# Kernel optimization log

Hardware: AMD Instinct MI355X
Metric: run time of the kernel (lower is better)

Reference implementation:

```python
import jax, jax.numpy as jnp
import numpy as np

B, T, D = 128, 1024, 128
HS = [100, 100, 200, 200]  # stacked LSTM hidden sizes (from initialize_carry calls)
OUT = 6


def _lstm_layer(xs, Wx, Wh, b):
    """Flax-style LSTMCell scanned over time. xs: [B,T,Din] -> [B,T,H].
    Gates: i,f,g,o ; c' = sig(f)*c + sig(i)*tanh(g) ; h' = sig(o)*tanh(c')."""
    Bsz = xs.shape[0]
    H = Wh.shape[0]
    c0 = jnp.zeros((Bsz, H), xs.dtype)
    h0 = jnp.zeros((Bsz, H), xs.dtype)

    def step(carry, x_t):
        c, h = carry
        z = x_t @ Wx + h @ Wh + b  # [B, 4H]
        i, f, g, o = jnp.split(z, 4, axis=-1)
        c = jax.nn.sigmoid(f) * c + jax.nn.sigmoid(i) * jnp.tanh(g)
        h = jax.nn.sigmoid(o) * jnp.tanh(c)
        return (c, h), h

    (_, _), hs = jax.lax.scan(step, (c0, h0), jnp.swapaxes(xs, 0, 1))  # hs: [T,B,H]
    return jnp.swapaxes(hs, 0, 1)


def setup_inputs() -> dict:
    key = jax.random.key(0)
    ks = jax.random.split(key, 16)
    xs = jax.random.normal(ks[0], (B, T, D), dtype=jnp.float32)
    inp = {"xs": xs}
    d_in = D
    for li, H in enumerate(HS):
        s_x = 1.0 / np.sqrt(d_in)
        s_h = 1.0 / np.sqrt(H)
        inp[f"Wx{li}"] = jax.random.normal(ks[1 + 3 * li], (d_in, 4 * H), dtype=jnp.float32) * s_x
        inp[f"Wh{li}"] = jax.random.normal(ks[2 + 3 * li], (H, 4 * H), dtype=jnp.float32) * s_h
        inp[f"b{li}"] = jnp.zeros((4 * H,), dtype=jnp.float32)
        d_in = H
    inp["Wd"] = jax.random.normal(ks[13], (HS[-1], OUT), dtype=jnp.float32) / np.sqrt(HS[-1])
    inp["bd"] = jnp.zeros((OUT,), dtype=jnp.float32)
    return inp


def reference(xs, Wx0, Wh0, b0, Wx1, Wh1, b1, Wx2, Wh2, b2, Wx3, Wh3, b3, Wd, bd):
    # Four stacked scanned LSTM layers (dropout is identity in eval mode)
    h = _lstm_layer(xs, Wx0, Wh0, b0)
    h = _lstm_layer(h, Wx1, Wh1, b1)
    h = _lstm_layer(h, Wx2, Wh2, b2)
    h = _lstm_layer(h, Wx3, Wh3, b3)
    last = h[:, -1, :]  # [B, 200]
    return last @ Wd + bd  # [B, 6]
```

## Files before the change

### kernel.cpp

```cpp
#include <hip/hip_runtime.h>
#include <cstdint>
#include <cstddef>


#define AGENT __HIP_MEMORY_SCOPE_AGENT
#define FSTR 64

typedef __attribute__((ext_vector_type(8))) short  short8;
typedef __attribute__((ext_vector_type(4))) float  f32x4;

struct us4 { unsigned short x, y, z, w; };

__device__ __forceinline__ unsigned short f2bf(float x){
  unsigned u = __float_as_uint(x);
  unsigned r = u + 0x7FFFu + ((u >> 16) & 1u);
  return (unsigned short)(r >> 16);
}
__device__ __forceinline__ float bf2f(unsigned short h){
  return __uint_as_float(((unsigned)h) << 16);
}
__device__ __forceinline__ float sigmoidf_(float x){ return 1.f / (1.f + __expf(-x)); }

__device__ __forceinline__ void spin_ge(const unsigned* p, unsigned v){
  #pragma unroll 1
  for (int i = 0; i < 32; ++i){
    if (__hip_atomic_load(p, __ATOMIC_RELAXED, AGENT) >= v) return;
  }
  long s = 0;
  #pragma unroll 1
  while (__hip_atomic_load(p, __ATOMIC_RELAXED, AGENT) < v){
    __builtin_amdgcn_s_sleep(8);
    if (++s > (1L << 17)) break;
  }
}

__device__ __forceinline__ void load_hx(const unsigned* base, int w32, int loOff,
                                        short8& ah, short8& al){
  union U { unsigned long long q[2]; short8 v; } uh, ul;
  const unsigned long long* ph = (const unsigned long long*)(base + w32);
  const unsigned long long* pl = (const unsigned long long*)(base + loOff + w32);
  uh.q[0] = __hip_atomic_load(ph + 0, __ATOMIC_RELAXED, AGENT);
  uh.q[1] = __hip_atomic_load(ph + 1, __ATOMIC_RELAXED, AGENT);
  ul.q[0] = __hip_atomic_load(pl + 0, __ATOMIC_RELAXED, AGENT);
  ul.q[1] = __hip_atomic_load(pl + 1, __ATOMIC_RELAXED, AGENT);
  ah = uh.v; al = ul.v;
}

__global__ __launch_bounds__(256) void gemm_pregate(
    const float* __restrict__ A, const float* __restrict__ W,
    const float* __restrict__ bias, float* __restrict__ G,
    int K, int KT, int N, size_t strideT, size_t strideB)
{
  __shared__ unsigned short Ahi[256*40];
  __shared__ unsigned short Alo[256*40];
  __shared__ unsigned short Bhi[80*40];
  __shared__ unsigned short Blo[80*40];

  const int tid  = threadIdx.x;
  const int mb   = blockIdx.x;
  const int n0   = blockIdx.y * 80;
  const int wave = tid >> 6, lane = tid & 63;
  const int ln15 = lane & 15, quad = lane >> 4;

  f32x4 acc[4][5];
  for (int a = 0; a < 4; ++a)
    for (int b = 0; b < 5; ++b)
      acc[a][b] = (f32x4){0.f, 0.f, 0.f, 0.f};

  for (int kt = 0; kt < KT; ++kt){
    const int k0 = kt * 32;
    const bool full = (k0 + 31) < K;
    for (int i = 0; i < 8; ++i){
      const int e   = tid + 256*i;
      const int row = e >> 3, seg = e & 7;
      const int mm  = mb*256 + row;
      const float* rp = A + (size_t)(mm >> 7)*strideT + (size_t)(mm & 127)*strideB;
      const int k = k0 + seg*4;
      float v0, v1, v2, v3;
      if (full){
        float4 v = *(const float4*)(rp + k);
        v0 = v.x; v1 = v.y; v2 = v.z; v3 = v.w;
      } else {
        v0 = (k+0 < K) ? rp[k+0] : 0.f;
        v1 = (k+1 < K) ? rp[k+1] : 0.f;
        v2 = (k+2 < K) ? rp[k+2] : 0.f;
        v3 = (k+3 < K) ? rp[k+3] : 0.f;
      }
      const unsigned short h0=f2bf(v0), h1=f2bf(v1), h2=f2bf(v2), h3=f2bf(v3);
      us4 hv{h0, h1, h2, h3};
      us4 lv{f2bf(v0-bf2f(h0)), f2bf(v1-bf2f(h1)), f2bf(v2-bf2f(h2)), f2bf(v3-bf2f(h3))};
      *(us4*)&Ahi[row*40 + seg*4] = hv;
      *(us4*)&Alo[row*40 + seg*4] = lv;
    }
    for (int i = 0; i < 10; ++i){
      const int e  = tid + 256*i;
      const int kk = e / 80, nn = e - kk*80;
      const int k  = k0 + kk;
      const float v = (k < K) ? W[(size_t)k*N + n0 + nn] : 0.f;
      const unsigned short hb = f2bf(v);
      Bhi[nn*40 + kk] = hb;
      Blo[nn*40 + kk] = f2bf(v - bf2f(hb));
    }
    __syncthreads();
    short8 a_h[4], a_l[4];
    for (int mt = 0; mt < 4; ++mt){
      const int aoff = (wave*64 + mt*16 + ln15)*40 + quad*8;
      a_h[mt] = *(const short8*)&Ahi[aoff];
      a_l[mt] = *(const short8*)&Alo[aoff];
    }
    for (int nt = 0; nt < 5; ++nt){
      const int boff = (nt*16 + ln15)*40 + quad*8;
      const short8 b_h = *(const short8*)&Bhi[boff];
      const short8 b_l = *(const short8*)&Blo[boff];
      for (int mt = 0; mt < 4; ++mt){
        acc[mt][nt] = __builtin_amdgcn_mfma_f32_16x16x32_bf16(a_h[mt], b_h, acc[mt][nt], 0,0,0);
        acc[mt][nt] = __builtin_amdgcn_mfma_f32_16x16x32_bf16(a_l[mt], b_h, acc[mt][nt], 0,0,0);
        acc[mt][nt] = __builtin_amdgcn_mfma_f32_16x16x32_bf16(a_h[mt], b_l, acc[mt][nt], 0,0,0);
      }
    }
    __syncthreads();
  }
  for (int nt = 0; nt < 5; ++nt){
    const float bv = bias[n0 + nt*16 + ln15];
    for (int mt = 0; mt < 4; ++mt){
      const int mbase = mb*256 + wave*64 + mt*16 + quad*4;
      #pragma unroll
      for (int r = 0; r < 4; ++r)
        G[(size_t)(mbase + r)*N + n0 + nt*16 + ln15] = acc[mt][nt][r] + bv;
    }
  }
}

template<int H, int HP, int P, bool HAS_X>
__device__ __forceinline__ void rec_stage(
    const float* __restrict__ G0, const float* __restrict__ Wx,
    const float* __restrict__ Wh, const float* __restrict__ bias,
    int HprevReal,
    const unsigned* __restrict__ HxUp, unsigned* __restrict__ HxOwn,
    const unsigned* __restrict__ flgUp, unsigned* __restrict__ flgOwn,
    unsigned* __restrict__ flgDn, int PUp, int PDn,
    float* __restrict__ cstate, float* __restrict__ hlast,
    int g, int m, int t0, int TC, int Tlast, char* smem)
{
  constexpr int HHM  = H / P;
  constexpr int COLS = 4 * HHM;
  constexpr int CP   = COLS;
  constexpr int ZSTR = CP + 1;
  constexpr int KPo  = ((H + 31)/32)*32;
  constexpr int RSo  = KPo / 2;
  constexpr int RSp  = HP / 2;
  constexpr int KX   = HAS_X ? HP : 0;
  constexpr int KALL = KX + KPo;
  constexpr int KTX  = KX / 32;
  constexpr int KTH  = KPo / 32;
  constexpr int KSTR = KALL + 8;
  constexpr int NT   = CP / 16;
  constexpr int NE   = 16 * HHM / 2;
  constexpr int PR   = HHM / 2;
  constexpr int N4H  = 4 * H;
  constexpr int SLOTo = 2*16*RSo;
  constexpr int SLOTp = 2*16*RSp;

  unsigned short* whT_hi = (unsigned short*)smem;
  unsigned short* whT_lo = whT_hi + CP*KSTR;
  float* zbuf = (float*)(whT_lo + CP*KSTR);

  const int tid  = threadIdx.x;
  const int row0 = g * 16;
  const int lane = tid & 63, wave = tid >> 6;
  const int ln15 = lane & 15, quad = lane >> 4;

  for (int e = tid; e < COLS*KALL; e += 256){
    const int k = e / COLS, c = e - k*COLS;
    const int gate = c / HHM, hh = c - gate*HHM;
    const int col = gate*H + m*HHM + hh;
    float w = 0.f;
    if (HAS_X){
      if (k < KX){ if (k < HprevReal) w = Wx[(size_t)k*N4H + col]; }
      else { const int k2 = k - KX; if (k2 < H) w = Wh[(size_t)k2*N4H + col]; }
    } else {
      if (k < H) w = Wh[(size_t)k*N4H + col];
    }
    const unsigned short hi = f2bf(w);
    whT_hi[c*KSTR + k] = hi;
    whT_lo[c*KSTR + k] = f2bf(w - bf2f(hi));
  }

  const int r_g  = tid / PR;
  const int hh0  = 2*(tid - r_g*PR);
  const int kidx = m*HHM + hh0;
  float c0 = 0.f, c1 = 0.f;
  if (tid < NE && t0 > 0){
    const float2 cv = *(const float2*)&cstate[(size_t)(row0 + r_g)*H + kidx];
    c0 = cv.x; c1 = cv.y;
  }
  float2 bv[4] = {};
  if (HAS_X){
    if (tid < NE){
      #pragma unroll
      for (int gate = 0; gate < 4; ++gate)
        bv[gate] = *(const float2*)&bias[gate*H + kidx];
    }
  }
  __syncthreads();

  const int g16 = g*16;

  for (int tl = 0; tl < TC; ++tl){
    const int t = t0 + tl;

    float2 gv[4] = {};
    if constexpr (!HAS_X){
      if (tid < NE){
        const float* Gt = G0 + ((size_t)tl*128 + row0 + r_g)*(size_t)N4H + kidx;
        #pragma unroll
        for (int gate = 0; gate < 4; ++gate)
          gv[gate] = *(const float2*)(Gt + gate*H);
      }
    }

    if (HAS_X && lane < PUp)
      spin_ge(&flgUp[(size_t)(g16 + lane)*FSTR], (unsigned)(t+1));
    __builtin_amdgcn_fence(__ATOMIC_ACQUIRE, "wavefront");

    f32x4 acc[2];
    acc[0] = (f32x4){0.f,0.f,0.f,0.f};
    acc[1] = (f32x4){0.f,0.f,0.f,0.f};
    auto do_tile = [&](const short8& a_h, const short8& a_l, int koW){
      #pragma unroll
      for (int s = 0; s < 2; ++s){
        const int nt = wave + 4*s;
        if (nt < NT){
          const int boff = (nt*16 + ln15)*KSTR + quad*8 + koW;
          const short8 b_h = *(const short8*)&whT_hi[boff];
          const short8 b_l = *(const short8*)&whT_lo[boff];
          acc[s] = __builtin_amdgcn_mfma_f32_16x16x32_bf16(a_h, b_h, acc[s], 0,0,0);
          acc[s] = __builtin_amdgcn_mfma_f32_16x16x32_bf16(a_l, b_h, acc[s], 0,0,0);
          acc[s] = __builtin_amdgcn_mfma_f32_16x16x32_bf16(a_h, b_l, acc[s], 0,0,0);
        }
      }
    };

    if constexpr (HAS_X){
      const unsigned* up = HxUp + ((size_t)(t & 7)*8 + g) * SLOTp;
      #pragma unroll
      for (int kt = 0; kt < KTX; ++kt){
        short8 a_h, a_l;
        load_hx(up, ln15*RSp + kt*16 + quad*4, 16*RSp, a_h, a_l);
        do_tile(a_h, a_l, kt*32);
      }
    }

    if (lane < P && lane != m)
      spin_ge(&flgOwn[(size_t)(g16 + lane)*FSTR], (unsigned)t);
    if (PDn > 0 && t >= 8 && lane >= 40 && lane < 40 + PDn)
      spin_ge(&flgDn[(size_t)(g16 + (lane-40))*FSTR], (unsigned)(t-7));
    __builtin_amdgcn_fence(__ATOMIC_ACQUIRE, "wavefront");

    {
      const unsigned* own = HxOwn + ((size_t)((t-1) & 7)*8 + g) * SLOTo;
      #pragma unroll
      for (int kt = 0; kt < KTH; ++kt){
        short8 a_h, a_l;
        load_hx(own, ln15*RSo + kt*16 + quad*4, 16*RSo, a_h, a_l);
        do_tile(a_h, a_l, KX + kt*32);
      }
    }
    {
      #pragma unroll
      for (int s = 0; s < 2; ++s){
        const int nt = wave + 4*s;
        if (nt < NT)
          #pragma unroll
          for (int r = 0; r < 4; ++r)
            zbuf[(quad*4 + r)*ZSTR + nt*16 + ln15] = acc[s][r];
      }
    }
    __syncthreads();

    if (tid < NE){
      const float* zr = zbuf + r_g*ZSTR;
      const float2 b0 = HAS_X ? bv[0] : gv[0];
      const float2 b1 = HAS_X ? bv[1] : gv[1];
      const float2 b2 = HAS_X ? bv[2] : gv[2];
      const float2 b3 = HAS_X ? bv[3] : gv[3];
      const float zi0 = zr[0*HHM + hh0]   + b0.x, zi1 = zr[0*HHM + hh0+1] + b0.y;
      const float zf0 = zr[1*HHM + hh0]   + b1.x, zf1 = zr[1*HHM + hh0+1] + b1.y;
      const float zg0 = zr[2*HHM + hh0]   + b2.x, zg1 = zr[2*HHM + hh0+1] + b2.y;
      const float zo0 = zr[3*HHM + hh0]   + b3.x, zo1 = zr[3*HHM + hh0+1] + b3.y;
      c0 = sigmoidf_(zf0)*c0 + sigmoidf_(zi0)*tanhf(zg0);
      c1 = sigmoidf_(zf1)*c1 + sigmoidf_(zi1)*tanhf(zg1);
      const float h0 = sigmoidf_(zo0)*tanhf(c0);
      const float h1 = sigmoidf_(zo1)*tanhf(c1);
      const unsigned short h0h = f2bf(h0), h1h = f2bf(h1);
      const unsigned short h0l = f2bf(h0 - bf2f(h0h)), h1l = f2bf(h1 - bf2f(h1h));
      const unsigned whi = ((unsigned)h1h << 16) | (unsigned)h0h;
      const unsigned wlo = ((unsigned)h1l << 16) | (unsigned)h0l;
      unsigned* dst = HxOwn + ((size_t)(t & 7)*8 + g) * SLOTo;
      const int w32 = r_g*RSo + (kidx >> 1);
      __hip_atomic_store(&dst[w32],          whi, __ATOMIC_RELAXED, AGENT);
      __hip_atomic_store(&dst[16*RSo + w32], wlo, __ATOMIC_RELAXED, AGENT);
      if (hlast && t == Tlast-1){
        float2 hv{h0, h1};
        *(float2*)&hlast[(size_t)(row0 + r_g)*H + kidx] = hv;
      }
    }
    __syncthreads();
    if (tid == 0)
      __hip_atomic_store(&flgOwn[(size_t)(g16 + m)*FSTR], (unsigned)(t+1),
                         __ATOMIC_RELAXED, AGENT);
  }

  if (tid < NE){
    float2 cv{c0, c1};
    *(float2*)&cstate[(size_t)(row0 + r_g)*H + kidx] = cv;
  }
}

struct FusedArgs {
  const float *G0;
  const float *Wx1, *Wx2, *Wx3;
  const float *Wh0, *Wh1, *Wh2, *Wh3;
  const float *b1, *b2, *b3;
  unsigned *Hx0, *Hx1, *Hx2, *Hx3;
  unsigned *flags;
  float *cst;
  float *hlast;
  int t0, TC, Tlast;
};

__global__ __launch_bounds__(256) void lstm_fused(FusedArgs a){
  extern __shared__ char smem[];
  const int b = blockIdx.x;
  constexpr int LF = 128*FSTR;
  if (b < 40){
    rec_stage<100, 0, 5, false>(a.G0, nullptr, a.Wh0, nullptr, 0,
        nullptr, a.Hx0, nullptr, a.flags + 0*LF, a.flags + 1*LF, 0, 5,
        a.cst + 0*128*200, nullptr, b & 7, b >> 3, a.t0, a.TC, a.Tlast, smem);
  } else if (b < 80){
    const int bb = b - 40;
    rec_stage<100, 128, 5, true>(nullptr, a.Wx1, a.Wh1, a.b1, 100,
        a.Hx0, a.Hx1, a.flags + 0*LF, a.flags + 1*LF, a.flags + 2*LF, 5, 10,
        a.cst + 1*128*200, nullptr, bb & 7, bb >> 3, a.t0, a.TC, a.Tlast, smem);
  } else if (b < 160){
    const int bb = b - 80;
    rec_stage<200, 128, 10, true>(nullptr, a.Wx2, a.Wh2, a.b2, 100,
        a.Hx1, a.Hx2, a.flags + 1*LF, a.flags + 2*LF, a.flags + 3*LF, 5, 10,
        a.cst + 2*128*200, nullptr, bb & 7, bb >> 3, a.t0, a.TC, a.Tlast, smem);
  } else {
    const int bb = b - 160;
    rec_stage<200, 224, 10, true>(nullptr, a.Wx3, a.Wh3, a.b3, 200,
        a.Hx2, a.Hx3, a.flags + 2*LF, a.flags + 3*LF, nullptr, 10, 0,
        a.cst + 3*128*200, a.hlast, bb & 7, bb >> 3, a.t0, a.TC, a.Tlast, smem);
  }
}

__global__ __launch_bounds__(256) void head_kernel(
    const float* __restrict__ hlast, const float* __restrict__ Wd,
    const float* __restrict__ bd, float* __restrict__ out)
{
  const int e = blockIdx.x*256 + threadIdx.x;
  if (e >= 128*6) return;
  const int b = e / 6, o = e - 6*b;
  float s = bd[o];
  const float* hp = hlast + (size_t)b*200;
  for (int k = 0; k < 200; ++k) s += hp[k] * Wd[k*6 + o];
  out[e] = s;
}

__global__ void fill_sentinel(float* out, int n){
  const int i = blockIdx.x*blockDim.x + threadIdx.x;
  if (i < n) out[i] = 1.0e30f;
}

extern "C" void kernel_launch(void* const* d_in, const int* in_sizes, int n_in,
                              void* d_out, int out_size, void* d_ws, size_t ws_size,
                              hipStream_t stream)
{
  (void)in_sizes; (void)n_in;
  const float* xs  = (const float*)d_in[0];
  const float* Wx[4] = {(const float*)d_in[1], (const float*)d_in[4],
                        (const float*)d_in[7], (const float*)d_in[10]};
  const float* Wh[4] = {(const float*)d_in[2], (const float*)d_in[5],
                        (const float*)d_in[8], (const float*)d_in[11]};
  const float* bs[4] = {(const float*)d_in[3], (const float*)d_in[6],
                        (const float*)d_in[9], (const float*)d_in[12]};
  const float* Wd = (const float*)d_in[13];
  const float* bd = (const float*)d_in[14];
  float* out = (float*)d_out;

  char* ws = (char*)d_ws;
  const size_t HXU[4] = {131072, 131072, 229376, 229376};
  const size_t HX_TOT = HXU[0]+HXU[1]+HXU[2]+HXU[3];
  const size_t FLAGS_BYTES = (size_t)4*128*FSTR*4;
  size_t off = 0;
  const size_t OFF_FLAGS = off; off += FLAGS_BYTES;
  const size_t OFF_HX    = off; off += HX_TOT*4;
  const size_t OFF_CST   = off; off += (size_t)4*128*200*4;
  const size_t OFF_HLAST = off; off += (size_t)128*200*4;
  off = (off + 255) & ~(size_t)255;
  const size_t FIXED_END = off;

  int CT = 0;
  for (int ct = 1024; ct >= 8; ct >>= 1){
    const size_t need = FIXED_END + (size_t)ct*128*400*4;
    if (ws_size >= need){ CT = ct; break; }
  }
  if (CT == 0){
    fill_sentinel<<<(out_size + 255)/256, 256, 0, stream>>>(out, out_size);
    return;
  }

  unsigned* flags = (unsigned*)(ws + OFF_FLAGS);
  unsigned* Hx0   = (unsigned*)(ws + OFF_HX);
  unsigned* Hx1   = Hx0 + HXU[0];
  unsigned* Hx2   = Hx1 + HXU[1];
  unsigned* Hx3   = Hx2 + HXU[2];
  float* cst      = (float*)(ws + OFF_CST);
  float* hlast    = (float*)(ws + OFF_HLAST);
  float* G0       = (float*)(ws + FIXED_END);

  const int FUSED_LDS = 151104;
  hipFuncSetAttribute(reinterpret_cast<const void*>(lstm_fused),
                      hipFuncAttributeMaxDynamicSharedMemorySize, FUSED_LDS);

  hipMemsetAsync(flags, 0, FLAGS_BYTES, stream);
  hipMemsetAsync(Hx0, 0, HX_TOT*4, stream);

  FusedArgs fa;
  fa.Wx1 = Wx[1]; fa.Wx2 = Wx[2]; fa.Wx3 = Wx[3];
  fa.Wh0 = Wh[0]; fa.Wh1 = Wh[1]; fa.Wh2 = Wh[2]; fa.Wh3 = Wh[3];
  fa.b1 = bs[1];  fa.b2 = bs[2];  fa.b3 = bs[3];
  fa.Hx0 = Hx0; fa.Hx1 = Hx1; fa.Hx2 = Hx2; fa.Hx3 = Hx3;
  fa.flags = flags; fa.cst = cst; fa.hlast = hlast;
  fa.G0 = G0; fa.Tlast = 1024;

  const int NC  = 1024 / CT;
  const int GMX = CT*128/256;
  for (int c = 0; c < NC; ++c){
    const int t0 = c*CT;
    gemm_pregate<<<dim3(GMX,5), 256, 0, stream>>>(xs + (size_t)t0*128, Wx[0], bs[0], G0,
        128, 4, 400, (size_t)128, (size_t)131072);
    fa.t0 = t0; fa.TC = CT;
    lstm_fused<<<240, 256, FUSED_LDS, stream>>>(fa);
  }

  head_kernel<<<3, 256, 0, stream>>>(hlast, Wd, bd, out);
}
```

Baseline: 6.474 ms.

## Merge per-step flag spins into one wave-wide wait and use fast tanh

Folds the three separate spin-waits (upstream layer, own peer blocks, downstream back-pressure) into a single per-lane spin whose pointer and offset are chosen once before the time loop, so all waits run concurrently instead of one after another. All A operands (upstream and own hidden state) are then loaded up front into register arrays before the MFMA loop. This loses the earlier overlap of upstream-input MFMAs with the wait on sibling blocks, and it raises register pressure. It also swaps tanhf for an exp-based formula, which is cheaper but slightly less accurate.

```diff
diff --git a/kernel.cpp b/kernel.cpp
--- a/kernel.cpp
+++ b/kernel.cpp
@@ -20,6 +20,9 @@
   return __uint_as_float(((unsigned)h) << 16);
 }
 __device__ __forceinline__ float sigmoidf_(float x){ return 1.f / (1.f + __expf(-x)); }
+__device__ __forceinline__ float tanhf_(float x){
+  return 1.f - 2.f / (1.f + __expf(2.f * x));
+}
 
 __device__ __forceinline__ void spin_ge(const unsigned* p, unsigned v){
   #pragma unroll 1
@@ -153,6 +156,7 @@
   constexpr int KALL = KX + KPo;
   constexpr int KTX  = KX / 32;
   constexpr int KTH  = KPo / 32;
+  constexpr int NTL  = KTX + KTH;
   constexpr int KSTR = KALL + 8;
   constexpr int NT   = CP / 16;
   constexpr int NE   = 16 * HHM / 2;
@@ -206,6 +210,18 @@
 
   const int g16 = g*16;
 
+  const unsigned* spin_p = nullptr;
+  int spin_dv = 0;
+  bool spin_bp = false;
+  if (HAS_X && lane < PUp){
+    spin_p = &flgUp[(size_t)(g16 + lane)*FSTR]; spin_dv = 1;
+  } else if (lane >= 16 && lane < 16 + P && (lane - 16) != m){
+    spin_p = &flgOwn[(size_t)(g16 + lane - 16)*FSTR]; spin_dv = 0;
+  } else if (PDn > 0 && lane >= 40 && lane < 40 + PDn){
+    spin_p = &flgDn[(size_t)(g16 + lane - 40)*FSTR]; spin_dv = -7;
+    spin_bp = true;
+  }
+
   for (int tl = 0; tl < TC; ++tl){
     const int t = t0 + tl;
 
@@ -219,62 +235,49 @@
       }
     }
 
-    if (HAS_X && lane < PUp)
-      spin_ge(&flgUp[(size_t)(g16 + lane)*FSTR], (unsigned)(t+1));
+    if (spin_p && !(spin_bp && t < 8))
+      spin_ge(spin_p, (unsigned)(t + spin_dv));
     __builtin_amdgcn_fence(__ATOMIC_ACQUIRE, "wavefront");
+
+    short8 ah[NTL], al[NTL];
+    if constexpr (HAS_X){
+      const unsigned* up = HxUp + ((size_t)(t & 7)*8 + g) * SLOTp;
+      #pragma unroll
+      for (int kt = 0; kt < KTX; ++kt)
+        load_hx(up, ln15*RSp + kt*16 + quad*4, 16*RSp, ah[kt], al[kt]);
+    }
+    {
+      const unsigned* own = HxOwn + ((size_t)((t-1) & 7)*8 + g) * SLOTo;
+      #pragma unroll
+      for (int kt = 0; kt < KTH; ++kt)
+        load_hx(own, ln15*RSo + kt*16 + quad*4, 16*RSo, ah[KTX+kt], al[KTX+kt]);
+    }
 
     f32x4 acc[2];
     acc[0] = (f32x4){0.f,0.f,0.f,0.f};
     acc[1] = (f32x4){0.f,0.f,0.f,0.f};
-    auto do_tile = [&](const short8& a_h, const short8& a_l, int koW){
+    #pragma unroll
+    for (int kt = 0; kt < NTL; ++kt){
       #pragma unroll
       for (int s = 0; s < 2; ++s){
         const int nt = wave + 4*s;
         if (nt < NT){
-          const int boff = (nt*16 + ln15)*KSTR + quad*8 + koW;
+          const int boff = (nt*16 + ln15)*KSTR + quad*8 + kt*32;
           const short8 b_h = *(const short8*)&whT_hi[boff];
           const short8 b_l = *(const short8*)&whT_lo[boff];
-          acc[s] = __builtin_amdgcn_mfma_f32_16x16x32_bf16(a_h, b_h, acc[s], 0,0,0);
-          acc[s] = __builtin_amdgcn_mfma_f32_16x16x32_bf16(a_l, b_h, acc[s], 0,0,0);
-          acc[s] = __builtin_amdgcn_mfma_f32_16x16x32_bf16(a_h, b_l, acc[s], 0,0,0);
+          acc[s] = __builtin_amdgcn_mfma_f32_16x16x32_bf16(ah[kt], b_h, acc[s], 0,0,0);
+          acc[s] = __builtin_amdgcn_mfma_f32_16x16x32_bf16(al[kt], b_h, acc[s], 0,0,0);
+          acc[s] = __builtin_amdgcn_mfma_f32_16x16x32_bf16(ah[kt], b_l, acc[s], 0,0,0);
         }
       }
-    };
-
-    if constexpr (HAS_X){
-      const unsigned* up = HxUp + ((size_t)(t & 7)*8 + g) * SLOTp;
-      #pragma unroll
-      for (int kt = 0; kt < KTX; ++kt){
-        short8 a_h, a_l;
-        load_hx(up, ln15*RSp + kt*16 + quad*4, 16*RSp, a_h, a_l);
-        do_tile(a_h, a_l, kt*32);
-      }
-    }
-
-    if (lane < P && lane != m)
-      spin_ge(&flgOwn[(size_t)(g16 + lane)*FSTR], (unsigned)t);
-    if (PDn > 0 && t >= 8 && lane >= 40 && lane < 40 + PDn)
-      spin_ge(&flgDn[(size_t)(g16 + (lane-40))*FSTR], (unsigned)(t-7));
-    __builtin_amdgcn_fence(__ATOMIC_ACQUIRE, "wavefront");
-
-    {
-      const unsigned* own = HxOwn + ((size_t)((t-1) & 7)*8 + g) * SLOTo;
-      #pragma unroll
-      for (int kt = 0; kt < KTH; ++kt){
-        short8 a_h, a_l;
-        load_hx(own, ln15*RSo + kt*16 + quad*4, 16*RSo, a_h, a_l);
-        do_tile(a_h, a_l, KX + kt*32);
-      }
-    }
-    {
-      #pragma unroll
-      for (int s = 0; s < 2; ++s){
-        const int nt = wave + 4*s;
-        if (nt < NT)
-          #pragma unroll
-          for (int r = 0; r < 4; ++r)
-            zbuf[(quad*4 + r)*ZSTR + nt*16 + ln15] = acc[s][r];
-      }
+    }
+    #pragma unroll
+    for (int s = 0; s < 2; ++s){
+      const int nt = wave + 4*s;
+      if (nt < NT)
+        #pragma unroll
+        for (int r = 0; r < 4; ++r)
+          zbuf[(quad*4 + r)*ZSTR + nt*16 + ln15] = acc[s][r];
     }
     __syncthreads();
 
@@ -288,10 +291,10 @@
       const float zf0 = zr[1*HHM + hh0]   + b1.x, zf1 = zr[1*HHM + hh0+1] + b1.y;
       const float zg0 = zr[2*HHM + hh0]   + b2.x, zg1 = zr[2*HHM + hh0+1] + b2.y;
       const float zo0 = zr[3*HHM + hh0]   + b3.x, zo1 = zr[3*HHM + hh0+1] + b3.y;
-      c0 = sigmoidf_(zf0)*c0 + sigmoidf_(zi0)*tanhf(zg0);
-      c1 = sigmoidf_(zf1)*c1 + sigmoidf_(zi1)*tanhf(zg1);
-      const float h0 = sigmoidf_(zo0)*tanhf(c0);
-      const float h1 = sigmoidf_(zo1)*tanhf(c1);
+      c0 = sigmoidf_(zf0)*c0 + sigmoidf_(zi0)*tanhf_(zg0);
+      c1 = sigmoidf_(zf1)*c1 + sigmoidf_(zi1)*tanhf_(zg1);
+      const float h0 = sigmoidf_(zo0)*tanhf_(c0);
+      const float h1 = sigmoidf_(zo1)*tanhf_(c1);
       const unsigned short h0h = f2bf(h0), h1h = f2bf(h1);
       const unsigned short h0l = f2bf(h0 - bf2f(h0h)), h1l = f2bf(h1 - bf2f(h1h));
       const unsigned whi = ((unsigned)h1h << 16) | (unsigned)h0h;
```

Result: slower. 7.491 ms (+15.7%).

## Replace per-block flags with per-group atomic counters and reorder recurrent MFMA before upstream wait

Applied to the files above, without the earlier changes.

Replaces the per-block step flags with one atomic counter per (layer, batch group), incremented by every producing block, so a single lane polls one counter instead of many lanes polling separate flags. The own-layer recurrent h·Wh tiles are now issued before waiting on the upstream and downstream counters, so that work can overlap the upstream layer's progress. The change also swaps tanhf for an exp-based fast tanh and shortens the spin sleep while raising the iteration cap. Risks include reduced tanh accuracy, memory-ordering subtleties since the atomics are relaxed, and counters that must be reset correctly across chunked launches.

```diff
diff --git a/kernel.cpp b/kernel.cpp
--- a/kernel.cpp
+++ b/kernel.cpp
@@ -20,6 +20,9 @@
   return __uint_as_float(((unsigned)h) << 16);
 }
 __device__ __forceinline__ float sigmoidf_(float x){ return 1.f / (1.f + __expf(-x)); }
+__device__ __forceinline__ float tanhf_(float x){
+  return 1.f - 2.f / (1.f + __expf(2.f * x));
+}
 
 __device__ __forceinline__ void spin_ge(const unsigned* p, unsigned v){
   #pragma unroll 1
@@ -29,8 +32,8 @@
   long s = 0;
   #pragma unroll 1
   while (__hip_atomic_load(p, __ATOMIC_RELAXED, AGENT) < v){
-    __builtin_amdgcn_s_sleep(8);
-    if (++s > (1L << 17)) break;
+    __builtin_amdgcn_s_sleep(2);
+    if (++s > (1L << 19)) break;
   }
 }
 
@@ -137,8 +140,8 @@
     const float* __restrict__ Wh, const float* __restrict__ bias,
     int HprevReal,
     const unsigned* __restrict__ HxUp, unsigned* __restrict__ HxOwn,
-    const unsigned* __restrict__ flgUp, unsigned* __restrict__ flgOwn,
-    unsigned* __restrict__ flgDn, int PUp, int PDn,
+    const unsigned* __restrict__ ctrUp, unsigned* __restrict__ ctrOwn,
+    const unsigned* __restrict__ ctrDn, int PUp, int PDn,
     float* __restrict__ cstate, float* __restrict__ hlast,
     int g, int m, int t0, int TC, int Tlast, char* smem)
 {
@@ -204,7 +207,12 @@
   }
   __syncthreads();
 
-  const int g16 = g*16;
+  const unsigned* cOwn = ctrOwn + (size_t)g*FSTR;
+  unsigned*       cOwnW = ctrOwn + (size_t)g*FSTR;
+  const unsigned* cUp  = HAS_X  ? (ctrUp + (size_t)g*FSTR) : nullptr;
+  const unsigned* cDn  = (PDn>0) ? (ctrDn + (size_t)g*FSTR) : nullptr;
+  const bool isUpLane = (HAS_X && lane == 0);
+  const bool isDnLane = (PDn > 0 && lane == 32);
 
   for (int tl = 0; tl < TC; ++tl){
     const int t = t0 + tl;
@@ -219,8 +227,8 @@
       }
     }
 
-    if (HAS_X && lane < PUp)
-      spin_ge(&flgUp[(size_t)(g16 + lane)*FSTR], (unsigned)(t+1));
+    if (lane == 0)
+      spin_ge(cOwn, (unsigned)(P * t));
     __builtin_amdgcn_fence(__ATOMIC_ACQUIRE, "wavefront");
 
     f32x4 acc[2];
@@ -241,6 +249,27 @@
       }
     };
 
+    {
+      const unsigned* own = HxOwn + ((size_t)((t-1) & 7)*8 + g) * SLOTo;
+      #pragma unroll
+      for (int kt = 0; kt < KTH; ++kt){
+        short8 a_h, a_l;
+        load_hx(own, ln15*RSo + kt*16 + quad*4, 16*RSo, a_h, a_l);
+        do_tile(a_h, a_l, KX + kt*32);
+      }
+    }
+
+    {
+      const bool act = (isUpLane) || (isDnLane && t >= 8);
+      if (act){
+        const unsigned* p2 = isUpLane ? cUp : cDn;
+        const unsigned tgt = isUpLane ? (unsigned)(PUp * (t+1))
+                                      : (unsigned)(PDn * (t-7));
+        spin_ge(p2, tgt);
+      }
+    }
+    __builtin_amdgcn_fence(__ATOMIC_ACQUIRE, "wavefront");
+
     if constexpr (HAS_X){
       const unsigned* up = HxUp + ((size_t)(t & 7)*8 + g) * SLOTp;
       #pragma unroll
@@ -251,21 +280,6 @@
       }
     }
 
-    if (lane < P && lane != m)
-      spin_ge(&flgOwn[(size_t)(g16 + lane)*FSTR], (unsigned)t);
-    if (PDn > 0 && t >= 8 && lane >= 40 && lane < 40 + PDn)
-      spin_ge(&flgDn[(size_t)(g16 + (lane-40))*FSTR], (unsigned)(t-7));
-    __builtin_amdgcn_fence(__ATOMIC_ACQUIRE, "wavefront");
-
-    {
-      const unsigned* own = HxOwn + ((size_t)((t-1) & 7)*8 + g) * SLOTo;
-      #pragma unroll
-      for (int kt = 0; kt < KTH; ++kt){
-        short8 a_h, a_l;
-        load_hx(own, ln15*RSo + kt*16 + quad*4, 16*RSo, a_h, a_l);
-        do_tile(a_h, a_l, KX + kt*32);
-      }
-    }
     {
       #pragma unroll
       for (int s = 0; s < 2; ++s){
@@ -288,10 +302,10 @@
       const float zf0 = zr[1*HHM + hh0]   + b1.x, zf1 = zr[1*HHM + hh0+1] + b1.y;
       const float zg0 = zr[2*HHM + hh0]   + b2.x, zg1 = zr[2*HHM + hh0+1] + b2.y;
       const float zo0 = zr[3*HHM + hh0]   + b3.x, zo1 = zr[3*HHM + hh0+1] + b3.y;
-      c0 = sigmoidf_(zf0)*c0 + sigmoidf_(zi0)*tanhf(zg0);
-      c1 = sigmoidf_(zf1)*c1 + sigmoidf_(zi1)*tanhf(zg1);
-      const float h0 = sigmoidf_(zo0)*tanhf(c0);
-      const float h1 = sigmoidf_(zo1)*tanhf(c1);
+      c0 = sigmoidf_(zf0)*c0 + sigmoidf_(zi0)*tanhf_(zg0);
+      c1 = sigmoidf_(zf1)*c1 + sigmoidf_(zi1)*tanhf_(zg1);
+      const float h0 = sigmoidf_(zo0)*tanhf_(c0);
+      const float h1 = sigmoidf_(zo1)*tanhf_(c1);
       const unsigned short h0h = f2bf(h0), h1h = f2bf(h1);
       const unsigned short h0l = f2bf(h0 - bf2f(h0h)), h1l = f2bf(h1 - bf2f(h1h));
       const unsigned whi = ((unsigned)h1h << 16) | (unsigned)h0h;
@@ -307,8 +321,7 @@
     }
     __syncthreads();
     if (tid == 0)
-      __hip_atomic_store(&flgOwn[(size_t)(g16 + m)*FSTR], (unsigned)(t+1),
-                         __ATOMIC_RELAXED, AGENT);
+      __hip_atomic_fetch_add(cOwnW, 1u, __ATOMIC_RELAXED, AGENT);
   }
 
   if (tid < NE){
@@ -332,25 +345,26 @@
 __global__ __launch_bounds__(256) void lstm_fused(FusedArgs a){
   extern __shared__ char smem[];
   const int b = blockIdx.x;
-  constexpr int LF = 128*FSTR;
+  constexpr int LF = 8*FSTR;
+  unsigned* F = a.flags;
   if (b < 40){
     rec_stage<100, 0, 5, false>(a.G0, nullptr, a.Wh0, nullptr, 0,
-        nullptr, a.Hx0, nullptr, a.flags + 0*LF, a.flags + 1*LF, 0, 5,
+        nullptr, a.Hx0, nullptr, F + 0*LF, F + 1*LF, 0, 5,
         a.cst + 0*128*200, nullptr, b & 7, b >> 3, a.t0, a.TC, a.Tlast, smem);
   } else if (b < 80){
     const int bb = b - 40;
     rec_stage<100, 128, 5, true>(nullptr, a.Wx1, a.Wh1, a.b1, 100,
-        a.Hx0, a.Hx1, a.flags + 0*LF, a.flags + 1*LF, a.flags + 2*LF, 5, 10,
+        a.Hx0, a.Hx1, F + 0*LF, F + 1*LF, F + 2*LF, 5, 10,
         a.cst + 1*128*200, nullptr, bb & 7, bb >> 3, a.t0, a.TC, a.Tlast, smem);
   } else if (b < 160){
     const int bb = b - 80;
     rec_stage<200, 128, 10, true>(nullptr, a.Wx2, a.Wh2, a.b2, 100,
-        a.Hx1, a.Hx2, a.flags + 1*LF, a.flags + 2*LF, a.flags + 3*LF, 5, 10,
+        a.Hx1, a.Hx2, F + 1*LF, F + 2*LF, F + 3*LF, 5, 10,
         a.cst + 2*128*200, nullptr, bb & 7, bb >> 3, a.t0, a.TC, a.Tlast, smem);
   } else {
     const int bb = b - 160;
     rec_stage<200, 224, 10, true>(nullptr, a.Wx3, a.Wh3, a.b3, 200,
-        a.Hx2, a.Hx3, a.flags + 2*LF, a.flags + 3*LF, nullptr, 10, 0,
+        a.Hx2, a.Hx3, F + 2*LF, F + 3*LF, nullptr, 10, 0,
         a.cst + 3*128*200, a.hlast, bb & 7, bb >> 3, a.t0, a.TC, a.Tlast, smem);
   }
 }
@@ -392,7 +406,7 @@
   char* ws = (char*)d_ws;
   const size_t HXU[4] = {131072, 131072, 229376, 229376};
   const size_t HX_TOT = HXU[0]+HXU[1]+HXU[2]+HXU[3];
-  const size_t FLAGS_BYTES = (size_t)4*128*FSTR*4;
+  const size_t FLAGS_BYTES = (size_t)4*8*FSTR*4;
   size_t off = 0;
   const size_t OFF_FLAGS = off; off += FLAGS_BYTES;
   const size_t OFF_HX    = off; off += HX_TOT*4;
```

Result: slower. 7.867 ms (+21.5%).

## Fuse layer-0 input projection into recurrent kernel, drop pregate GEMM

Applied to the files above, without the earlier changes.

Removes the separate pregate GEMM for layer 0. Layer-0 blocks now load xs directly each timestep, split it into bf16 hi/lo parts and multiply by Wx0 held in LDS alongside Wh0, which leaves a single fused launch over all 1024 steps with no G0 workspace. It also replaces tanhf with an exp-based tanh. This avoids the extra kernel, the G0 write/read traffic and any chunking, at the cost of more per-step work and global xs loads on layer 0's critical path.

```diff
diff --git a/kernel.cpp b/kernel.cpp
--- a/kernel.cpp
+++ b/kernel.cpp
@@ -8,8 +8,6 @@
 
 typedef __attribute__((ext_vector_type(8))) short  short8;
 typedef __attribute__((ext_vector_type(4))) float  f32x4;
-
-struct us4 { unsigned short x, y, z, w; };
 
 __device__ __forceinline__ unsigned short f2bf(float x){
   unsigned u = __float_as_uint(x);
@@ -20,6 +18,9 @@
   return __uint_as_float(((unsigned)h) << 16);
 }
 __device__ __forceinline__ float sigmoidf_(float x){ return 1.f / (1.f + __expf(-x)); }
+__device__ __forceinline__ float tanhf_(float x){
+  return 1.f - 2.f / (1.f + __expf(2.f * x));
+}
 
 __device__ __forceinline__ void spin_ge(const unsigned* p, unsigned v){
   #pragma unroll 1
@@ -46,96 +47,11 @@
   ah = uh.v; al = ul.v;
 }
 
-__global__ __launch_bounds__(256) void gemm_pregate(
-    const float* __restrict__ A, const float* __restrict__ W,
-    const float* __restrict__ bias, float* __restrict__ G,
-    int K, int KT, int N, size_t strideT, size_t strideB)
-{
-  __shared__ unsigned short Ahi[256*40];
-  __shared__ unsigned short Alo[256*40];
-  __shared__ unsigned short Bhi[80*40];
-  __shared__ unsigned short Blo[80*40];
-
-  const int tid  = threadIdx.x;
-  const int mb   = blockIdx.x;
-  const int n0   = blockIdx.y * 80;
-  const int wave = tid >> 6, lane = tid & 63;
-  const int ln15 = lane & 15, quad = lane >> 4;
-
-  f32x4 acc[4][5];
-  for (int a = 0; a < 4; ++a)
-    for (int b = 0; b < 5; ++b)
-      acc[a][b] = (f32x4){0.f, 0.f, 0.f, 0.f};
-
-  for (int kt = 0; kt < KT; ++kt){
-    const int k0 = kt * 32;
-    const bool full = (k0 + 31) < K;
-    for (int i = 0; i < 8; ++i){
-      const int e   = tid + 256*i;
-      const int row = e >> 3, seg = e & 7;
-      const int mm  = mb*256 + row;
-      const float* rp = A + (size_t)(mm >> 7)*strideT + (size_t)(mm & 127)*strideB;
-      const int k = k0 + seg*4;
-      float v0, v1, v2, v3;
-      if (full){
-        float4 v = *(const float4*)(rp + k);
-        v0 = v.x; v1 = v.y; v2 = v.z; v3 = v.w;
-      } else {
-        v0 = (k+0 < K) ? rp[k+0] : 0.f;
-        v1 = (k+1 < K) ? rp[k+1] : 0.f;
-        v2 = (k+2 < K) ? rp[k+2] : 0.f;
-        v3 = (k+3 < K) ? rp[k+3] : 0.f;
-      }
-      const unsigned short h0=f2bf(v0), h1=f2bf(v1), h2=f2bf(v2), h3=f2bf(v3);
-      us4 hv{h0, h1, h2, h3};
-      us4 lv{f2bf(v0-bf2f(h0)), f2bf(v1-bf2f(h1)), f2bf(v2-bf2f(h2)), f2bf(v3-bf2f(h3))};
-      *(us4*)&Ahi[row*40 + seg*4] = hv;
-      *(us4*)&Alo[row*40 + seg*4] = lv;
-    }
-    for (int i = 0; i < 10; ++i){
-      const int e  = tid + 256*i;
-      const int kk = e / 80, nn = e - kk*80;
-      const int k  = k0 + kk;
-      const float v = (k < K) ? W[(size_t)k*N + n0 + nn] : 0.f;
-      const unsigned short hb = f2bf(v);
-      Bhi[nn*40 + kk] = hb;
-      Blo[nn*40 + kk] = f2bf(v - bf2f(hb));
-    }
-    __syncthreads();
-    short8 a_h[4], a_l[4];
-    for (int mt = 0; mt < 4; ++mt){
-      const int aoff = (wave*64 + mt*16 + ln15)*40 + quad*8;
-      a_h[mt] = *(const short8*)&Ahi[aoff];
-      a_l[mt] = *(const short8*)&Alo[aoff];
-    }
-    for (int nt = 0; nt < 5; ++nt){
-      const int boff = (nt*16 + ln15)*40 + quad*8;
-      const short8 b_h = *(const short8*)&Bhi[boff];
-      const short8 b_l = *(const short8*)&Blo[boff];
-      for (int mt = 0; mt < 4; ++mt){
-        acc[mt][nt] = __builtin_amdgcn_mfma_f32_16x16x32_bf16(a_h[mt], b_h, acc[mt][nt], 0,0,0);
-        acc[mt][nt] = __builtin_amdgcn_mfma_f32_16x16x32_bf16(a_l[mt], b_h, acc[mt][nt], 0,0,0);
-        acc[mt][nt] = __builtin_amdgcn_mfma_f32_16x16x32_bf16(a_h[mt], b_l, acc[mt][nt], 0,0,0);
-      }
-    }
-    __syncthreads();
-  }
-  for (int nt = 0; nt < 5; ++nt){
-    const float bv = bias[n0 + nt*16 + ln15];
-    for (int mt = 0; mt < 4; ++mt){
-      const int mbase = mb*256 + wave*64 + mt*16 + quad*4;
-      #pragma unroll
-      for (int r = 0; r < 4; ++r)
-        G[(size_t)(mbase + r)*N + n0 + nt*16 + ln15] = acc[mt][nt][r] + bv;
-    }
-  }
-}
-
-template<int H, int HP, int P, bool HAS_X>
+template<int H, int HP, int P, bool XS_IN>
 __device__ __forceinline__ void rec_stage(
-    const float* __restrict__ G0, const float* __restrict__ Wx,
-    const float* __restrict__ Wh, const float* __restrict__ bias,
-    int HprevReal,
+    const float* __restrict__ xs,
+    const float* __restrict__ Wx, const float* __restrict__ Wh,
+    const float* __restrict__ bias, int HprevReal,
     const unsigned* __restrict__ HxUp, unsigned* __restrict__ HxOwn,
     const unsigned* __restrict__ flgUp, unsigned* __restrict__ flgOwn,
     unsigned* __restrict__ flgDn, int PUp, int PDn,
@@ -144,17 +60,16 @@
 {
   constexpr int HHM  = H / P;
   constexpr int COLS = 4 * HHM;
-  constexpr int CP   = COLS;
-  constexpr int ZSTR = CP + 1;
+  constexpr int ZSTR = COLS + 1;
   constexpr int KPo  = ((H + 31)/32)*32;
   constexpr int RSo  = KPo / 2;
   constexpr int RSp  = HP / 2;
-  constexpr int KX   = HAS_X ? HP : 0;
+  constexpr int KX   = HP;
   constexpr int KALL = KX + KPo;
   constexpr int KTX  = KX / 32;
   constexpr int KTH  = KPo / 32;
   constexpr int KSTR = KALL + 8;
-  constexpr int NT   = CP / 16;
+  constexpr int NT   = COLS / 16;
   constexpr int NE   = 16 * HHM / 2;
   constexpr int PR   = HHM / 2;
   constexpr int N4H  = 4 * H;
@@ -162,8 +77,8 @@
   constexpr int SLOTp = 2*16*RSp;
 
   unsigned short* whT_hi = (unsigned short*)smem;
-  unsigned short* whT_lo = whT_hi + CP*KSTR;
-  float* zbuf = (float*)(whT_lo + CP*KSTR);
+  unsigned short* whT_lo = whT_hi + COLS*KSTR;
+  float* zbuf = (float*)(whT_lo + COLS*KSTR);
 
   const int tid  = threadIdx.x;
   const int row0 = g * 16;
@@ -175,12 +90,8 @@
     const int gate = c / HHM, hh = c - gate*HHM;
     const int col = gate*H + m*HHM + hh;
     float w = 0.f;
-    if (HAS_X){
-      if (k < KX){ if (k < HprevReal) w = Wx[(size_t)k*N4H + col]; }
-      else { const int k2 = k - KX; if (k2 < H) w = Wh[(size_t)k2*N4H + col]; }
-    } else {
-      if (k < H) w = Wh[(size_t)k*N4H + col];
-    }
+    if (k < KX){ if (k < HprevReal) w = Wx[(size_t)k*N4H + col]; }
+    else { const int k2 = k - KX; if (k2 < H) w = Wh[(size_t)k2*N4H + col]; }
     const unsigned short hi = f2bf(w);
     whT_hi[c*KSTR + k] = hi;
     whT_lo[c*KSTR + k] = f2bf(w - bf2f(hi));
@@ -195,12 +106,10 @@
     c0 = cv.x; c1 = cv.y;
   }
   float2 bv[4] = {};
-  if (HAS_X){
-    if (tid < NE){
-      #pragma unroll
-      for (int gate = 0; gate < 4; ++gate)
-        bv[gate] = *(const float2*)&bias[gate*H + kidx];
-    }
+  if (tid < NE){
+    #pragma unroll
+    for (int gate = 0; gate < 4; ++gate)
+      bv[gate] = *(const float2*)&bias[gate*H + kidx];
   }
   __syncthreads();
 
@@ -209,19 +118,11 @@
   for (int tl = 0; tl < TC; ++tl){
     const int t = t0 + tl;
 
-    float2 gv[4] = {};
-    if constexpr (!HAS_X){
-      if (tid < NE){
-        const float* Gt = G0 + ((size_t)tl*128 + row0 + r_g)*(size_t)N4H + kidx;
-        #pragma unroll
-        for (int gate = 0; gate < 4; ++gate)
-          gv[gate] = *(const float2*)(Gt + gate*H);
-      }
-    }
-
-    if (HAS_X && lane < PUp)
-      spin_ge(&flgUp[(size_t)(g16 + lane)*FSTR], (unsigned)(t+1));
-    __builtin_amdgcn_fence(__ATOMIC_ACQUIRE, "wavefront");
+    if constexpr (!XS_IN){
+      if (lane < PUp)
+        spin_ge(&flgUp[(size_t)(g16 + lane)*FSTR], (unsigned)(t+1));
+      __builtin_amdgcn_fence(__ATOMIC_ACQUIRE, "wavefront");
+    }
 
     f32x4 acc[2];
     acc[0] = (f32x4){0.f,0.f,0.f,0.f};
@@ -241,7 +142,24 @@
       }
     };
 
-    if constexpr (HAS_X){
+    if constexpr (XS_IN){
+      const float* xp = xs + (size_t)(row0 + ln15)*(1024*128)
+                           + (size_t)t*128 + quad*8;
+      #pragma unroll
+      for (int kt = 0; kt < KTX; ++kt){
+        const float4 v0 = *(const float4*)(xp + kt*32);
+        const float4 v1 = *(const float4*)(xp + kt*32 + 4);
+        const float xv[8] = {v0.x, v0.y, v0.z, v0.w, v1.x, v1.y, v1.z, v1.w};
+        union SU { unsigned short u[8]; short8 v; } sh, sl;
+        #pragma unroll
+        for (int j = 0; j < 8; ++j){
+          const unsigned short hi = f2bf(xv[j]);
+          sh.u[j] = hi;
+          sl.u[j] = f2bf(xv[j] - bf2f(hi));
+        }
+        do_tile(sh.v, sl.v, kt*32);
+      }
+    } else {
       const unsigned* up = HxUp + ((size_t)(t & 7)*8 + g) * SLOTp;
       #pragma unroll
       for (int kt = 0; kt < KTX; ++kt){
@@ -280,18 +198,14 @@
 
     if (tid < NE){
       const float* zr = zbuf + r_g*ZSTR;
-      const float2 b0 = HAS_X ? bv[0] : gv[0];
-      const float2 b1 = HAS_X ? bv[1] : gv[1];
-      const float2 b2 = HAS_X ? bv[2] : gv[2];
-      const float2 b3 = HAS_X ? bv[3] : gv[3];
-      const float zi0 = zr[0*HHM + hh0]   + b0.x, zi1 = zr[0*HHM + hh0+1] + b0.y;
-      const float zf0 = zr[1*HHM + hh0]   + b1.x, zf1 = zr[1*HHM + hh0+1] + b1.y;
-      const float zg0 = zr[2*HHM + hh0]   + b2.x, zg1 = zr[2*HHM + hh0+1] + b2.y;
-      const float zo0 = zr[3*HHM + hh0]   + b3.x, zo1 = zr[3*HHM + hh0+1] + b3.y;
-      c0 = sigmoidf_(zf0)*c0 + sigmoidf_(zi0)*tanhf(zg0);
-      c1 = sigmoidf_(zf1)*c1 + sigmoidf_(zi1)*tanhf(zg1);
-      const float h0 = sigmoidf_(zo0)*tanhf(c0);
-      const float h1 = sigmoidf_(zo1)*tanhf(c1);
+      const float zi0 = zr[0*HHM + hh0]   + bv[0].x, zi1 = zr[0*HHM + hh0+1] + bv[0].y;
+      const float zf0 = zr[1*HHM + hh0]   + bv[1].x, zf1 = zr[1*HHM + hh0+1] + bv[1].y;
+      const float zg0 = zr[2*HHM + hh0]   + bv[2].x, zg1 = zr[2*HHM + hh0+1] + bv[2].y;
+      const float zo0 = zr[3*HHM + hh0]   + bv[3].x, zo1 = zr[3*HHM + hh0+1] + bv[3].y;
+      c0 = sigmoidf_(zf0)*c0 + sigmoidf_(zi0)*tanhf_(zg0);
+      c1 = sigmoidf_(zf1)*c1 + sigmoidf_(zi1)*tanhf_(zg1);
+      const float h0 = sigmoidf_(zo0)*tanhf_(c0);
+      const float h1 = sigmoidf_(zo1)*tanhf_(c1);
       const unsigned short h0h = f2bf(h0), h1h = f2bf(h1);
       const unsigned short h0l = f2bf(h0 - bf2f(h0h)), h1l = f2bf(h1 - bf2f(h1h));
       const unsigned whi = ((unsigned)h1h << 16) | (unsigned)h0h;
@@ -318,10 +232,10 @@
 }
 
 struct FusedArgs {
-  const float *G0;
-  const float *Wx1, *Wx2, *Wx3;
+  const float *xs;
+  const float *Wx0, *Wx1, *Wx2, *Wx3;
   const float *Wh0, *Wh1, *Wh2, *Wh3;
-  const float *b1, *b2, *b3;
+  const float *b0, *b1, *b2, *b3;
   unsigned *Hx0, *Hx1, *Hx2, *Hx3;
   unsigned *flags;
   float *cst;
@@ -333,24 +247,25 @@
   extern __shared__ char smem[];
   const int b = blockIdx.x;
   constexpr int LF = 128*FSTR;
+  unsigned* F = a.flags;
   if (b < 40){
-    rec_stage<100, 0, 5, false>(a.G0, nullptr, a.Wh0, nullptr, 0,
-        nullptr, a.Hx0, nullptr, a.flags + 0*LF, a.flags + 1*LF, 0, 5,
+    rec_stage<100, 128, 5, true>(a.xs, a.Wx0, a.Wh0, a.b0, 128,
+        nullptr, a.Hx0, nullptr, F + 0*LF, F + 1*LF, 0, 5,
         a.cst + 0*128*200, nullptr, b & 7, b >> 3, a.t0, a.TC, a.Tlast, smem);
   } else if (b < 80){
     const int bb = b - 40;
-    rec_stage<100, 128, 5, true>(nullptr, a.Wx1, a.Wh1, a.b1, 100,
-        a.Hx0, a.Hx1, a.flags + 0*LF, a.flags + 1*LF, a.flags + 2*LF, 5, 10,
+    rec_stage<100, 128, 5, false>(nullptr, a.Wx1, a.Wh1, a.b1, 100,
+        a.Hx0, a.Hx1, F + 0*LF, F + 1*LF, F + 2*LF, 5, 10,
         a.cst + 1*128*200, nullptr, bb & 7, bb >> 3, a.t0, a.TC, a.Tlast, smem);
   } else if (b < 160){
     const int bb = b - 80;
-    rec_stage<200, 128, 10, true>(nullptr, a.Wx2, a.Wh2, a.b2, 100,
-        a.Hx1, a.Hx2, a.flags + 1*LF, a.flags + 2*LF, a.flags + 3*LF, 5, 10,
+    rec_stage<200, 128, 10, false>(nullptr, a.Wx2, a.Wh2, a.b2, 100,
+        a.Hx1, a.Hx2, F + 1*LF, F + 2*LF, F + 3*LF, 5, 10,
         a.cst + 2*128*200, nullptr, bb & 7, bb >> 3, a.t0, a.TC, a.Tlast, smem);
   } else {
     const int bb = b - 160;
-    rec_stage<200, 224, 10, true>(nullptr, a.Wx3, a.Wh3, a.b3, 200,
-        a.Hx2, a.Hx3, a.flags + 2*LF, a.flags + 3*LF, nullptr, 10, 0,
+    rec_stage<200, 224, 10, false>(nullptr, a.Wx3, a.Wh3, a.b3, 200,
+        a.Hx2, a.Hx3, F + 2*LF, F + 3*LF, nullptr, 10, 0,
         a.cst + 3*128*200, a.hlast, bb & 7, bb >> 3, a.t0, a.TC, a.Tlast, smem);
   }
 }
@@ -399,14 +314,8 @@
   const size_t OFF_CST   = off; off += (size_t)4*128*200*4;
   const size_t OFF_HLAST = off; off += (size_t)128*200*4;
   off = (off + 255) & ~(size_t)255;
-  const size_t FIXED_END = off;
-
-  int CT = 0;
-  for (int ct = 1024; ct >= 8; ct >>= 1){
-    const size_t need = FIXED_END + (size_t)ct*128*400*4;
-    if (ws_size >= need){ CT = ct; break; }
-  }
-  if (CT == 0){
+
+  if (ws_size < off){
     fill_sentinel<<<(out_size + 255)/256, 256, 0, stream>>>(out, out_size);
     return;
   }
@@ -418,7 +327,6 @@
   unsigned* Hx3   = Hx2 + HXU[2];
   float* cst      = (float*)(ws + OFF_CST);
   float* hlast    = (float*)(ws + OFF_HLAST);
-  float* G0       = (float*)(ws + FIXED_END);
 
   const int FUSED_LDS = 151104;
   hipFuncSetAttribute(reinterpret_cast<const void*>(lstm_fused),
@@ -428,22 +336,15 @@
   hipMemsetAsync(Hx0, 0, HX_TOT*4, stream);
 
   FusedArgs fa;
-  fa.Wx1 = Wx[1]; fa.Wx2 = Wx[2]; fa.Wx3 = Wx[3];
+  fa.xs = xs;
+  fa.Wx0 = Wx[0]; fa.Wx1 = Wx[1]; fa.Wx2 = Wx[2]; fa.Wx3 = Wx[3];
   fa.Wh0 = Wh[0]; fa.Wh1 = Wh[1]; fa.Wh2 = Wh[2]; fa.Wh3 = Wh[3];
-  fa.b1 = bs[1];  fa.b2 = bs[2];  fa.b3 = bs[3];
+  fa.b0 = bs[0];  fa.b1 = bs[1];  fa.b2 = bs[2];  fa.b3 = bs[3];
   fa.Hx0 = Hx0; fa.Hx1 = Hx1; fa.Hx2 = Hx2; fa.Hx3 = Hx3;
   fa.flags = flags; fa.cst = cst; fa.hlast = hlast;
-  fa.G0 = G0; fa.Tlast = 1024;
-
-  const int NC  = 1024 / CT;
-  const int GMX = CT*128/256;
-  for (int c = 0; c < NC; ++c){
-    const int t0 = c*CT;
-    gemm_pregate<<<dim3(GMX,5), 256, 0, stream>>>(xs + (size_t)t0*128, Wx[0], bs[0], G0,
-        128, 4, 400, (size_t)128, (size_t)131072);
-    fa.t0 = t0; fa.TC = CT;
-    lstm_fused<<<240, 256, FUSED_LDS, stream>>>(fa);
-  }
+  fa.t0 = 0; fa.TC = 1024; fa.Tlast = 1024;
+
+  lstm_fused<<<240, 256, FUSED_LDS, stream>>>(fa);
 
   head_kernel<<<3, 256, 0, stream>>>(hlast, Wd, bd, out);
 }
```

After: 6.086 ms. 1.06x faster.
